# Kernel optimization log

Hardware: AMD Instinct MI355X
Metric: run time of the kernel (lower is better)

The kernel has to match this reference:

```python
import jax, jax.numpy as jnp
import numpy as np

N = 50000
E = 1600000

def _glorot(k, shp):
    lim = np.sqrt(6.0 / (shp[0] + shp[1])).astype(np.float32)
    return jax.random.uniform(k, shp, jnp.float32, -lim, lim)

def setup_inputs() -> dict:
    key = jax.random.key(0)
    ks = jax.random.split(key, 8)
    return {
        "x": jax.random.normal(ks[0], (N, 640), jnp.float32),
        "edges": jax.random.randint(ks[1], (E, 2), 0, N),  # [E,2] (src, dst)
        "Wb": _glorot(ks[2], (640, 64)),  "bb": jnp.zeros((64,), jnp.float32),
        "Ws1": _glorot(ks[3], (64, 64)),  "bs1": jnp.zeros((64,), jnp.float32),
        "Ws2": _glorot(ks[4], (64, 640)), "bs2": jnp.zeros((640,), jnp.float32),
        "Ww1": _glorot(ks[5], (64, 64)),  "bw1": jnp.zeros((64,), jnp.float32),
        "Ww2": _glorot(ks[6], (64, 640)), "bw2": jnp.zeros((640,), jnp.float32),
    }

def _gcn_conv(x, W, b, src, dst, dinv):
    # PyG GCNConv: x' = D^{-1/2}(A+I)D^{-1/2} x W + b (self-loops included)
    h = x @ W  # [N, out]
    coef = dinv[src] * dinv[dst]  # symmetric norm per edge
    agg = jax.ops.segment_sum(h[src] * coef[:, None], dst, num_segments=x.shape[0])
    agg = agg + h * (dinv * dinv)[:, None]  # self-loop contribution
    return agg + b

def reference(x, edges, Wb, bb, Ws1, bs1, Ws2, bs2, Ww1, bw1, Ww2, bw2):
    src, dst = edges[:, 0], edges[:, 1]
    # degree includes the added self-loop
    deg = jax.ops.segment_sum(jnp.ones_like(dst, jnp.float32), dst, num_segments=x.shape[0]) + 1.0
    dinv = jax.lax.rsqrt(deg)
    xb = jax.nn.relu(_gcn_conv(x, Wb, bb, src, dst, dinv))
    xs = jax.nn.relu(_gcn_conv(xb, Ws1, bs1, src, dst, dinv))
    xs = jax.nn.relu(_gcn_conv(xs, Ws2, bs2, src, dst, dinv))
    xw = jax.nn.relu(_gcn_conv(xb, Ww1, bw1, src, dst, dinv))
    xw = jax.nn.relu(_gcn_conv(xw, Ww2, bw2, src, dst, dinv))
    return (xs, xw)
```

## Files before the change

### kernel.cpp

```cpp
#include <hip/hip_runtime.h>


__global__ void zero_int_kernel(int* __restrict__ p, int n) {
    int i = blockIdx.x * blockDim.x + threadIdx.x;
    if (i < n) p[i] = 0;
}

__global__ void hist_kernel(const int* __restrict__ edges, int* __restrict__ cnt, int E) {
    int e = blockIdx.x * blockDim.x + threadIdx.x;
    if (e < E) atomicAdd(&cnt[edges[2 * e + 1]], 1);
}

__global__ __launch_bounds__(1024)
void scan_block_kernel(const int* __restrict__ cnt, int* __restrict__ excl,
                       int* __restrict__ blocksum, float* __restrict__ dinv, int N) {
    __shared__ int s[1024];
    int tid = threadIdx.x;
    int i = blockIdx.x * 1024 + tid;
    int v = (i < N) ? cnt[i] : 0;
    if (i < N) dinv[i] = rsqrtf((float)v + 1.0f);
    s[tid] = v;
    __syncthreads();
    for (int off = 1; off < 1024; off <<= 1) {
        int t = (tid >= off) ? s[tid - off] : 0;
        __syncthreads();
        s[tid] += t;
        __syncthreads();
    }
    if (i < N) excl[i] = s[tid] - v;
    if (tid == 1023) blocksum[blockIdx.x] = s[1023];
}

__global__ void scan_partials_kernel(int* __restrict__ blocksum, int nb) {
    if (blockIdx.x == 0 && threadIdx.x == 0) {
        int run = 0;
        for (int i = 0; i < nb; ++i) { int v = blocksum[i]; blocksum[i] = run; run += v; }
    }
}

__global__ void scan_finalize_kernel(int* __restrict__ row_start, const int* __restrict__ blocksum,
                                     int* __restrict__ cursor, int N, int E) {
    int i = blockIdx.x * blockDim.x + threadIdx.x;
    if (i < N) {
        int v = row_start[i] + blocksum[i >> 10];
        row_start[i] = v;
        cursor[i] = v;
    }
    if (i == N) row_start[N] = E;
}

__global__ void build_csr_kernel(const int* __restrict__ edges, int* __restrict__ cursor,
                                 int* __restrict__ csr_src, int E) {
    int e = blockIdx.x * blockDim.x + threadIdx.x;
    if (e < E) {
        int s = edges[2 * e], d = edges[2 * e + 1];
        int pos = atomicAdd(&cursor[d], 1);
        csr_src[pos] = s;
    }
}

template <bool BIAS, bool RELU>
__global__ __launch_bounds__(256)
void agg_gather_kernel(const float* __restrict__ in, const float* __restrict__ bias,
                       const int* __restrict__ row_start, const int* __restrict__ csr_src,
                       const float* __restrict__ dinv, float* __restrict__ out, int N) {
    int lane = threadIdx.x & 63;
    int wid  = (blockIdx.x * blockDim.x + threadIdx.x) >> 6;
    int nw   = (gridDim.x * blockDim.x) >> 6;
    float b = BIAS ? bias[lane] : 0.f;
    for (int d = wid; d < N; d += nw) {
        float dv = dinv[d];
        float v = in[(size_t)d * 64 + lane];
        if (BIAS) v += b;
        if (RELU) v = fmaxf(v, 0.f);
        float acc0 = v * dv * dv;
        float acc1 = 0.f;
        int e   = row_start[d];
        int end = row_start[d + 1];
        for (; e + 1 < end; e += 2) {
            int s0 = csr_src[e], s1 = csr_src[e + 1];
            float c0 = dinv[s0] * dv, c1 = dinv[s1] * dv;
            float u0 = in[(size_t)s0 * 64 + lane];
            float u1 = in[(size_t)s1 * 64 + lane];
            if (BIAS) { u0 += b; u1 += b; }
            if (RELU) { u0 = fmaxf(u0, 0.f); u1 = fmaxf(u1, 0.f); }
            acc0 = fmaf(u0, c0, acc0);
            acc1 = fmaf(u1, c1, acc1);
        }
        if (e < end) {
            int s0 = csr_src[e];
            float c0 = dinv[s0] * dv;
            float u0 = in[(size_t)s0 * 64 + lane];
            if (BIAS) u0 += b;
            if (RELU) u0 = fmaxf(u0, 0.f);
            acc0 = fmaf(u0, c0, acc0);
        }
        out[(size_t)d * 64 + lane] = acc0 + acc1;
    }
}

template <bool RELU>
__global__ __launch_bounds__(256)
void gemm_kernel(const float* __restrict__ A, const float* __restrict__ B,
                 const float* __restrict__ bias, float* __restrict__ C,
                 int M, int N, int K) {
    __shared__ float sA[64][33];
    __shared__ float sB[32][64];
    const int tid  = threadIdx.x;
    const int row0 = blockIdx.x * 64;
    const int col0 = blockIdx.y * 64;
    const int tx = tid & 15;
    const int ty = tid >> 4;
    const int tx4 = tx << 2, ty4 = ty << 2;

    float acc[4][4] = {};

    for (int kb = 0; kb < K; kb += 32) {
#pragma unroll
        for (int l = 0; l < 2; ++l) {
            int f  = tid + l * 256;
            int r  = f >> 3;
            int k4 = (f & 7) << 2;
            float4 v = make_float4(0.f, 0.f, 0.f, 0.f);
            int gr = row0 + r;
            if (gr < M) v = *(const float4*)&A[(size_t)gr * K + kb + k4];
            sA[r][k4 + 0] = v.x; sA[r][k4 + 1] = v.y;
            sA[r][k4 + 2] = v.z; sA[r][k4 + 3] = v.w;
        }
#pragma unroll
        for (int l = 0; l < 2; ++l) {
            int f  = tid + l * 256;
            int kr = f >> 4;
            int c4 = (f & 15) << 2;
            *(float4*)&sB[kr][c4] = *(const float4*)&B[(size_t)(kb + kr) * N + col0 + c4];
        }
        __syncthreads();
#pragma unroll
        for (int k = 0; k < 32; ++k) {
            float a0 = sA[ty4 + 0][k];
            float a1 = sA[ty4 + 1][k];
            float a2 = sA[ty4 + 2][k];
            float a3 = sA[ty4 + 3][k];
            float4 b = *(const float4*)&sB[k][tx4];
            acc[0][0] = fmaf(a0, b.x, acc[0][0]); acc[0][1] = fmaf(a0, b.y, acc[0][1]);
            acc[0][2] = fmaf(a0, b.z, acc[0][2]); acc[0][3] = fmaf(a0, b.w, acc[0][3]);
            acc[1][0] = fmaf(a1, b.x, acc[1][0]); acc[1][1] = fmaf(a1, b.y, acc[1][1]);
            acc[1][2] = fmaf(a1, b.z, acc[1][2]); acc[1][3] = fmaf(a1, b.w, acc[1][3]);
            acc[2][0] = fmaf(a2, b.x, acc[2][0]); acc[2][1] = fmaf(a2, b.y, acc[2][1]);
            acc[2][2] = fmaf(a2, b.z, acc[2][2]); acc[2][3] = fmaf(a2, b.w, acc[2][3]);
            acc[3][0] = fmaf(a3, b.x, acc[3][0]); acc[3][1] = fmaf(a3, b.y, acc[3][1]);
            acc[3][2] = fmaf(a3, b.z, acc[3][2]); acc[3][3] = fmaf(a3, b.w, acc[3][3]);
        }
        __syncthreads();
    }

    float4 bv = make_float4(0.f, 0.f, 0.f, 0.f);
    if (bias) bv = *(const float4*)&bias[col0 + tx4];
#pragma unroll
    for (int i = 0; i < 4; ++i) {
        int gr = row0 + ty4 + i;
        if (gr < M) {
            float4 v;
            v.x = acc[i][0] + bv.x; v.y = acc[i][1] + bv.y;
            v.z = acc[i][2] + bv.z; v.w = acc[i][3] + bv.w;
            if (RELU) {
                v.x = fmaxf(v.x, 0.f); v.y = fmaxf(v.y, 0.f);
                v.z = fmaxf(v.z, 0.f); v.w = fmaxf(v.w, 0.f);
            }
            *(float4*)&C[(size_t)gr * N + col0 + tx4] = v;
        }
    }
}

extern "C" void kernel_launch(void* const* d_in, const int* in_sizes, int n_in,
                              void* d_out, int out_size, void* d_ws, size_t ws_size,
                              hipStream_t stream) {
    const float* x     = (const float*)d_in[0];
    const int*   edges = (const int*)d_in[1];
    const float* Wb    = (const float*)d_in[2];
    const float* bb    = (const float*)d_in[3];
    const float* Ws1   = (const float*)d_in[4];
    const float* bs1   = (const float*)d_in[5];
    const float* Ws2   = (const float*)d_in[6];
    const float* bs2   = (const float*)d_in[7];
    const float* Ww1   = (const float*)d_in[8];
    const float* bw1   = (const float*)d_in[9];
    const float* Ww2   = (const float*)d_in[10];
    const float* bw2   = (const float*)d_in[11];

    const int N = in_sizes[0] / 640;
    const int E = in_sizes[1] / 2;

    float* out_xs = (float*)d_out;
    float* out_xw = out_xs + (size_t)N * 640;

    const size_t NP = ((size_t)N + 64) & ~63ULL;
    char* w = (char*)d_ws;
    float* dinv      = (float*)w;              w += NP * 4;
    int*   cnt       = (int*)w;                w += NP * 4;
    int*   row_start = (int*)w;                w += (NP + 64) * 4;
    int*   cursor    = (int*)w;                w += NP * 4;
    int*   csr_src   = (int*)w;                w += ((size_t)E + 64) * 4;
    size_t nf = (size_t)N * 64;
    float* B0 = (float*)w;                     w += nf * 4;
    float* B1 = (float*)w;                     w += nf * 4;
    float* B2 = (float*)w;                     w += nf * 4;

    const dim3 blk(256);
    const int nBlkN   = (N + 255) / 256;
    const int nBlkN1  = (N + 256) / 256;
    const int nBlkE   = (E + 255) / 256;
    const int nScanB  = (N + 1023) / 1024;
    const int rowT    = (N + 63) / 64;
    const int gatherB = (N + 3) / 4;

    zero_int_kernel<<<nBlkN, blk, 0, stream>>>(cnt, N);
    hist_kernel<<<nBlkE, blk, 0, stream>>>(edges, cnt, E);
    scan_block_kernel<<<nScanB, 1024, 0, stream>>>(cnt, row_start, cursor , dinv, N);
    scan_partials_kernel<<<1, 64, 0, stream>>>(cursor, nScanB);
    scan_finalize_kernel<<<nBlkN1, blk, 0, stream>>>(row_start, cursor, cnt , N, E);
    build_csr_kernel<<<nBlkE, blk, 0, stream>>>(edges, cnt, csr_src, E);

    gemm_kernel<false><<<dim3(rowT, 1), blk, 0, stream>>>(x, Wb, nullptr, B0, N, 64, 640);

    agg_gather_kernel<false, false><<<gatherB, blk, 0, stream>>>(B0, nullptr, row_start, csr_src, dinv, B1, N);

    agg_gather_kernel<true, true><<<gatherB, blk, 0, stream>>>(B1, bb, row_start, csr_src, dinv, B2, N);

    gemm_kernel<true><<<dim3(rowT, 1), blk, 0, stream>>>(B2, Ws1, bs1, B0, N, 64, 64);
    agg_gather_kernel<false, false><<<gatherB, blk, 0, stream>>>(B0, nullptr, row_start, csr_src, dinv, B1, N);
    gemm_kernel<true><<<dim3(rowT, 10), blk, 0, stream>>>(B1, Ws2, bs2, out_xs, N, 640, 64);

    gemm_kernel<true><<<dim3(rowT, 1), blk, 0, stream>>>(B2, Ww1, bw1, B0, N, 64, 64);
    agg_gather_kernel<false, false><<<gatherB, blk, 0, stream>>>(B0, nullptr, row_start, csr_src, dinv, B1, N);
    gemm_kernel<true><<<dim3(rowT, 10), blk, 0, stream>>>(B1, Ww2, bw2, out_xw, N, 640, 64);
}
```

Baseline: 1.059 ms.

## Precompute edge norm coefficients and merge the two branch aggregations into one 128-wide pass

The CSR build now stores the per-edge normalization coefficient next to the source index, so the gather kernels no longer do a random dinv lookup per edge. The two 64-wide branch GEMMs (Ws1, Ww1) are merged into a single 128-wide GEMM over concatenated weights. Their two aggregations are replaced by one 128-wide gather that reads float2 per lane, so the CSR is traversed once instead of twice. The final GEMMs read strided halves of the combined buffer. The cost is doubled CSR storage, an extra small concat kernel, larger workspace, and a 4-way unrolled 64-wide gather.

Measured after the change: 900.2 us (median of 3 runs). -15.0%, faster.

```diff
diff --git a/kernel.cpp b/kernel.cpp
--- a/kernel.cpp
+++ b/kernel.cpp
@@ -50,20 +50,33 @@
 }
 
 __global__ void build_csr_kernel(const int* __restrict__ edges, int* __restrict__ cursor,
-                                 int* __restrict__ csr_src, int E) {
+                                 int2* __restrict__ csr, const float* __restrict__ dinv, int E) {
     int e = blockIdx.x * blockDim.x + threadIdx.x;
     if (e < E) {
         int s = edges[2 * e], d = edges[2 * e + 1];
+        float c = dinv[s] * dinv[d];
         int pos = atomicAdd(&cursor[d], 1);
-        csr_src[pos] = s;
-    }
+        csr[pos] = make_int2(s, __float_as_int(c));
+    }
+}
+
+__global__ void concat_w_kernel(const float* __restrict__ Ws1, const float* __restrict__ Ww1,
+                                const float* __restrict__ bs1, const float* __restrict__ bw1,
+                                float* __restrict__ Wcat, float* __restrict__ bcat) {
+    int i = blockIdx.x * blockDim.x + threadIdx.x;
+    if (i < 4096) {
+        int k = i >> 6, c = i & 63;
+        Wcat[k * 128 + c]       = Ws1[i];
+        Wcat[k * 128 + 64 + c]  = Ww1[i];
+    }
+    if (i < 64) { bcat[i] = bs1[i]; bcat[64 + i] = bw1[i]; }
 }
 
 template <bool BIAS, bool RELU>
 __global__ __launch_bounds__(256)
-void agg_gather_kernel(const float* __restrict__ in, const float* __restrict__ bias,
-                       const int* __restrict__ row_start, const int* __restrict__ csr_src,
-                       const float* __restrict__ dinv, float* __restrict__ out, int N) {
+void agg64_kernel(const float* __restrict__ in, const float* __restrict__ bias,
+                  const int* __restrict__ row_start, const int2* __restrict__ csr,
+                  const float* __restrict__ dinv, float* __restrict__ out, int N) {
     int lane = threadIdx.x & 63;
     int wid  = (blockIdx.x * blockDim.x + threadIdx.x) >> 6;
     int nw   = (gridDim.x * blockDim.x) >> 6;
@@ -74,28 +87,65 @@
         if (BIAS) v += b;
         if (RELU) v = fmaxf(v, 0.f);
         float acc0 = v * dv * dv;
-        float acc1 = 0.f;
+        float acc1 = 0.f, acc2 = 0.f, acc3 = 0.f;
+        int e   = row_start[d];
+        int end = row_start[d + 1];
+        for (; e + 3 < end; e += 4) {
+            int2 r0 = csr[e + 0], r1 = csr[e + 1], r2 = csr[e + 2], r3 = csr[e + 3];
+            float u0 = in[(size_t)r0.x * 64 + lane];
+            float u1 = in[(size_t)r1.x * 64 + lane];
+            float u2 = in[(size_t)r2.x * 64 + lane];
+            float u3 = in[(size_t)r3.x * 64 + lane];
+            if (BIAS) { u0 += b; u1 += b; u2 += b; u3 += b; }
+            if (RELU) {
+                u0 = fmaxf(u0, 0.f); u1 = fmaxf(u1, 0.f);
+                u2 = fmaxf(u2, 0.f); u3 = fmaxf(u3, 0.f);
+            }
+            acc0 = fmaf(u0, __int_as_float(r0.y), acc0);
+            acc1 = fmaf(u1, __int_as_float(r1.y), acc1);
+            acc2 = fmaf(u2, __int_as_float(r2.y), acc2);
+            acc3 = fmaf(u3, __int_as_float(r3.y), acc3);
+        }
+        for (; e < end; ++e) {
+            int2 r = csr[e];
+            float u = in[(size_t)r.x * 64 + lane];
+            if (BIAS) u += b;
+            if (RELU) u = fmaxf(u, 0.f);
+            acc0 = fmaf(u, __int_as_float(r.y), acc0);
+        }
+        out[(size_t)d * 64 + lane] = (acc0 + acc1) + (acc2 + acc3);
+    }
+}
+
+__global__ __launch_bounds__(256)
+void agg128_kernel(const float* __restrict__ in, const int* __restrict__ row_start,
+                   const int2* __restrict__ csr, const float* __restrict__ dinv,
+                   float* __restrict__ out, int N) {
+    int lane = threadIdx.x & 63;
+    int wid  = (blockIdx.x * blockDim.x + threadIdx.x) >> 6;
+    int nw   = (gridDim.x * blockDim.x) >> 6;
+    for (int d = wid; d < N; d += nw) {
+        float dv = dinv[d];
+        float2 v = *(const float2*)&in[(size_t)d * 128 + lane * 2];
+        float aA = v.x * dv * dv, bA = v.y * dv * dv;
+        float aB = 0.f, bB = 0.f;
         int e   = row_start[d];
         int end = row_start[d + 1];
         for (; e + 1 < end; e += 2) {
-            int s0 = csr_src[e], s1 = csr_src[e + 1];
-            float c0 = dinv[s0] * dv, c1 = dinv[s1] * dv;
-            float u0 = in[(size_t)s0 * 64 + lane];
-            float u1 = in[(size_t)s1 * 64 + lane];
-            if (BIAS) { u0 += b; u1 += b; }
-            if (RELU) { u0 = fmaxf(u0, 0.f); u1 = fmaxf(u1, 0.f); }
-            acc0 = fmaf(u0, c0, acc0);
-            acc1 = fmaf(u1, c1, acc1);
+            int2 r0 = csr[e], r1 = csr[e + 1];
+            float2 u0 = *(const float2*)&in[(size_t)r0.x * 128 + lane * 2];
+            float2 u1 = *(const float2*)&in[(size_t)r1.x * 128 + lane * 2];
+            float c0 = __int_as_float(r0.y), c1 = __int_as_float(r1.y);
+            aA = fmaf(u0.x, c0, aA); bA = fmaf(u0.y, c0, bA);
+            aB = fmaf(u1.x, c1, aB); bB = fmaf(u1.y, c1, bB);
         }
         if (e < end) {
-            int s0 = csr_src[e];
-            float c0 = dinv[s0] * dv;
-            float u0 = in[(size_t)s0 * 64 + lane];
-            if (BIAS) u0 += b;
-            if (RELU) u0 = fmaxf(u0, 0.f);
-            acc0 = fmaf(u0, c0, acc0);
-        }
-        out[(size_t)d * 64 + lane] = acc0 + acc1;
+            int2 r = csr[e];
+            float2 u = *(const float2*)&in[(size_t)r.x * 128 + lane * 2];
+            float c = __int_as_float(r.y);
+            aA = fmaf(u.x, c, aA); bA = fmaf(u.y, c, bA);
+        }
+        *(float2*)&out[(size_t)d * 128 + lane * 2] = make_float2(aA + aB, bA + bB);
     }
 }
 
@@ -103,7 +153,7 @@
 __global__ __launch_bounds__(256)
 void gemm_kernel(const float* __restrict__ A, const float* __restrict__ B,
                  const float* __restrict__ bias, float* __restrict__ C,
-                 int M, int N, int K) {
+                 int M, int N, int K, int lda) {
     __shared__ float sA[64][33];
     __shared__ float sB[32][64];
     const int tid  = threadIdx.x;
@@ -123,7 +173,7 @@
             int k4 = (f & 7) << 2;
             float4 v = make_float4(0.f, 0.f, 0.f, 0.f);
             int gr = row0 + r;
-            if (gr < M) v = *(const float4*)&A[(size_t)gr * K + kb + k4];
+            if (gr < M) v = *(const float4*)&A[(size_t)gr * lda + kb + k4];
             sA[r][k4 + 0] = v.x; sA[r][k4 + 1] = v.y;
             sA[r][k4 + 2] = v.z; sA[r][k4 + 3] = v.w;
         }
@@ -200,11 +250,15 @@
     int*   cnt       = (int*)w;                w += NP * 4;
     int*   row_start = (int*)w;                w += (NP + 64) * 4;
     int*   cursor    = (int*)w;                w += NP * 4;
-    int*   csr_src   = (int*)w;                w += ((size_t)E + 64) * 4;
+    int2*  csr       = (int2*)w;               w += ((size_t)E + 64) * 8;
+    float* Wcat      = (float*)w;              w += 8192 * 4;
+    float* bcat      = (float*)w;              w += 256 * 4;
     size_t nf = (size_t)N * 64;
     float* B0 = (float*)w;                     w += nf * 4;
     float* B1 = (float*)w;                     w += nf * 4;
     float* B2 = (float*)w;                     w += nf * 4;
+    float* Bcat = (float*)w;                   w += (size_t)N * 128 * 4;
+    float* B128 = (float*)w;                   w += (size_t)N * 128 * 4;
 
     const dim3 blk(256);
     const int nBlkN   = (N + 255) / 256;
@@ -219,19 +273,20 @@
     scan_block_kernel<<<nScanB, 1024, 0, stream>>>(cnt, row_start, cursor , dinv, N);
     scan_partials_kernel<<<1, 64, 0, stream>>>(cursor, nScanB);
     scan_finalize_kernel<<<nBlkN1, blk, 0, stream>>>(row_start, cursor, cnt , N, E);
-    build_csr_kernel<<<nBlkE, blk, 0, stream>>>(edges, cnt, csr_src, E);
-
-    gemm_kernel<false><<<dim3(rowT, 1), blk, 0, stream>>>(x, Wb, nullptr, B0, N, 64, 640);
-
-    agg_gather_kernel<false, false><<<gatherB, blk, 0, stream>>>(B0, nullptr, row_start, csr_src, dinv, B1, N);
-
-    agg_gather_kernel<true, true><<<gatherB, blk, 0, stream>>>(B1, bb, row_start, csr_src, dinv, B2, N);
-
-    gemm_kernel<true><<<dim3(rowT, 1), blk, 0, stream>>>(B2, Ws1, bs1, B0, N, 64, 64);
-    agg_gather_kernel<false, false><<<gatherB, blk, 0, stream>>>(B0, nullptr, row_start, csr_src, dinv, B1, N);
-    gemm_kernel<true><<<dim3(rowT, 10), blk, 0, stream>>>(B1, Ws2, bs2, out_xs, N, 640, 64);
-
-    gemm_kernel<true><<<dim3(rowT, 1), blk, 0, stream>>>(B2, Ww1, bw1, B0, N, 64, 64);
-    agg_gather_kernel<false, false><<<gatherB, blk, 0, stream>>>(B0, nullptr, row_start, csr_src, dinv, B1, N);
-    gemm_kernel<true><<<dim3(rowT, 10), blk, 0, stream>>>(B1, Ww2, bw2, out_xw, N, 640, 64);
-}
+    build_csr_kernel<<<nBlkE, blk, 0, stream>>>(edges, cnt, csr, dinv, E);
+
+    concat_w_kernel<<<16, blk, 0, stream>>>(Ws1, Ww1, bs1, bw1, Wcat, bcat);
+
+    gemm_kernel<false><<<dim3(rowT, 1), blk, 0, stream>>>(x, Wb, nullptr, B0, N, 64, 640, 640);
+
+    agg64_kernel<false, false><<<gatherB, blk, 0, stream>>>(B0, nullptr, row_start, csr, dinv, B1, N);
+
+    agg64_kernel<true, true><<<gatherB, blk, 0, stream>>>(B1, bb, row_start, csr, dinv, B2, N);
+
+    gemm_kernel<true><<<dim3(rowT, 2), blk, 0, stream>>>(B2, Wcat, bcat, Bcat, N, 128, 64, 64);
+
+    agg128_kernel<<<gatherB, blk, 0, stream>>>(Bcat, row_start, csr, dinv, B128, N);
+
+    gemm_kernel<true><<<dim3(rowT, 10), blk, 0, stream>>>(B128,      Ws2, bs2, out_xs, N, 640, 64, 128);
+    gemm_kernel<true><<<dim3(rowT, 10), blk, 0, stream>>>(B128 + 64, Ww2, bw2, out_xw, N, 640, 64, 128);
+}
```
